# Performance work log

Hardware: AMD Instinct MI355X
Metric: run time of the kernel (lower is better)

The kernel has to match this reference:

```python
import jax, jax.numpy as jnp
import numpy as np

S = 128           # seq_len
B = 256           # input_bits (bits per token, also neurons per head)
H = 16            # num_heads
NB = 12           # n_bits_per_neuron -> LUT size 2^12
PB = 7            # relative-position bits = ceil(log2(max_seq_len))
HEAD_IN = 2 * B + PB   # concat(query, key, rel_pos_bits) = 519
THRESH = H // 2


def setup_inputs() -> dict:
    key = jax.random.key(0)
    k1, k2, k3 = jax.random.split(key, 3)
    tokens = jax.random.randint(k1, (S, B), 0, 2, dtype=jnp.int32)           # binary token bits
    memory = jax.random.normal(k2, (H, B, 2 ** NB), dtype=jnp.float32)       # RAM LUT contents per head/neuron
    connections = jax.random.randint(k3, (H, B, NB), 0, HEAD_IN, dtype=jnp.int32)  # per-neuron input-bit wiring
    return {"tokens": tokens, "memory": memory, "connections": connections}


def reference(tokens, memory, connections):
    idx = jnp.arange(S)
    rel = idx[:, None] - idx[None, :]                         # [S,S] i - j
    mask = (rel >= 0).astype(jnp.int32)                        # causal mask (j <= i)
    relc = jnp.clip(rel, 0, S - 1)
    # relative-distance binary encoding, LSB first: [S,S,PB]
    pos_bits = ((relc[..., None] >> jnp.arange(PB)) & 1).astype(jnp.int32)
    q = jnp.broadcast_to(tokens[:, None, :], (S, S, B))
    k = jnp.broadcast_to(tokens[None, :, :], (S, S, B))
    head_in = jnp.concatenate([q, k, pos_bits], axis=-1)       # [S,S,HEAD_IN]
    # RAM address per (query i, key j, head h, neuron n): pack NB wired bits, LSB first
    addr = jnp.zeros((S, S, H, B), dtype=jnp.int32)
    for b in range(NB):  # tiny fixed loop over bit planes, fully vectorized over S,S,H,B
        addr = addr + (head_in[..., connections[:, :, b]] << b)
    # LUT gather: memory[h, n, addr] -> [S,S,H,B]
    h_idx = jnp.arange(H)[:, None]
    n_idx = jnp.arange(B)[None, :]
    vals = memory[h_idx, n_idx, addr]
    bits = (vals > 0.0).astype(jnp.int32)                      # RAM neuron output bit
    # XOR accumulation over attended keys == masked sum mod 2: [S,H,B]
    head_res = jnp.sum(bits * mask[:, :, None, None], axis=1) % 2
    # majority vote across heads per bit
    ones_count = jnp.sum(head_res, axis=1)                     # [S,B]
    return (ones_count > THRESH).astype(jnp.int32)
```

## Files before the change

### kernel.cpp

```cpp
#include <hip/hip_runtime.h>
#include <hip/hip_bf16.h>


#define S 128
#define B 256
#define H 16
#define NB 12

typedef __attribute__((address_space(3))) void       lds_void;
typedef const __attribute__((address_space(1))) void glb_void;

__device__ __forceinline__ void async16(const float* g, float* l) {
    __builtin_amdgcn_global_load_lds((glb_void*)g, (lds_void*)l, 16, 0, 0);
}

__global__ __launch_bounds__(1024) void softram_kernel(
    const int* __restrict__ tokens,
    const float* __restrict__ memory,
    const int* __restrict__ connections,
    int* __restrict__ out)
{
    const int n    = blockIdx.x;
    const int tid  = threadIdx.x;
    const int wv   = tid >> 6;
    const int lane = tid & 63;

    __shared__ float          raw[2][2][4096];
    __shared__ unsigned int   tok[S * 8];
    __shared__ unsigned short aqs[H][S];
    __shared__ unsigned short aks[H][S];
    __shared__ unsigned short aps[H][S];
    __shared__ int            conns[H][NB];
    __shared__ int            hasP[H];
    __shared__ unsigned char  partsA[H][8];
    __shared__ unsigned char  partsB[H][8];

    auto issue_round = [&](int r, int buf) {
        #pragma unroll
        for (int q2 = 0; q2 < 2; ++q2) {
            int c = wv * 2 + q2;
            const float* g = memory + ((size_t)((2 * r + (c >> 4)) * 256 + n) << 12)
                           + ((c & 15) << 8) + (lane << 2);
            float* l = &raw[buf][c >> 4][(c & 15) << 8];
            async16(g, l);
        }
    };

    issue_round(0, 0);
    {
        int i = tid >> 3, w = tid & 7;
        const int4* tp = (const int4*)tokens;
        unsigned int t = 0;
        #pragma unroll
        for (int u = 0; u < 8; ++u) {
            int4 x = tp[i * 64 + w * 8 + u];
            t |= (unsigned)(x.x & 1) << (4 * u + 0);
            t |= (unsigned)(x.y & 1) << (4 * u + 1);
            t |= (unsigned)(x.z & 1) << (4 * u + 2);
            t |= (unsigned)(x.w & 1) << (4 * u + 3);
        }
        tok[tid] = t;
    }
    if (tid < H * NB) {
        int h = tid / NB, b = tid - h * NB;
        conns[h][b] = connections[h * (B * NB) + n * NB + b];
    }
    __syncthreads();

    issue_round(1, 1);

    if (tid < H) {
        int f = 0;
        #pragma unroll
        for (int b = 0; b < NB; ++b) f |= (conns[tid][b] >= 512);
        hasP[tid] = f;
    }
    #pragma unroll
    for (int e0 = 0; e0 < 2; ++e0) {
        int e = tid + (e0 << 10);
        int h = e >> 7, ii = e & 127;
        unsigned aq = 0, ak = 0, ap = 0;
        #pragma unroll
        for (int b = 0; b < NB; ++b) {
            int c = conns[h][b];
            if (c < 256) {
                aq |= ((tok[ii * 8 + (c >> 5)] >> (c & 31)) & 1u) << b;
            } else if (c < 512) {
                int c2 = c - 256;
                ak |= ((tok[ii * 8 + (c2 >> 5)] >> (c2 & 31)) & 1u) << b;
            } else {
                ap |= (unsigned)((ii >> (c - 512)) & 1) << b;
            }
        }
        aqs[h][ii] = (unsigned short)aq;
        aks[h][ii] = (unsigned short)ak;
        aps[h][ii] = (unsigned short)ap;
    }
    __syncthreads();

    const int hh = wv & 1;
    const int q  = wv >> 1;
    for (int r = 0; r < 8; ++r) {
        if (r < 7) issue_round(r + 1, (r + 1) & 1);

        const int h = 2 * r + hh;
        const float* __restrict__ lrow = &raw[r & 1][hh][0];
        const unsigned ak0 = aks[h][lane];
        const unsigned ak1 = aks[h][lane + 64];
        const bool hp = (hasP[h] != 0);
        unsigned accA = 0, accB = 0;

        {
            uint4 aqw = *(const uint4*)&aqs[h][q * 8];
            const unsigned short* aqp = (const unsigned short*)&aqw;
            #pragma unroll
            for (int t = 0; t < 8; ++t) {
                int i = q * 8 + t;
                unsigned ap0 = hp ? (unsigned)aps[h][(i - lane) & 127] : 0u;
                float v0 = lrow[aqp[t] + ak0 + ap0];
                unsigned long long m0 = __ballot(v0 > 0.0f);
                unsigned long long c0 = (2ull << i) - 1;
                accA |= (unsigned)(__popcll(m0 & c0) & 1) << t;
            }
        }
        {
            uint4 aqw = *(const uint4*)&aqs[h][64 + q * 8];
            const unsigned short* aqp = (const unsigned short*)&aqw;
            #pragma unroll
            for (int t = 0; t < 8; ++t) {
                int i = 64 + q * 8 + t;
                unsigned ap0 = 0, ap1 = 0;
                if (hp) {
                    ap0 = aps[h][(i - lane) & 127];
                    ap1 = aps[h][(i - lane - 64) & 127];
                }
                float v0 = lrow[aqp[t] + ak0 + ap0];
                float v1 = lrow[aqp[t] + ak1 + ap1];
                unsigned long long m0 = __ballot(v0 > 0.0f);
                unsigned long long m1 = __ballot(v1 > 0.0f);
                unsigned long long c1 = (2ull << (i - 64)) - 1;
                accB |= (unsigned)((__popcll(m0) + __popcll(m1 & c1)) & 1) << t;
            }
        }
        if (lane == 0) {
            partsA[h][q] = (unsigned char)accA;
            partsB[h][q] = (unsigned char)accB;
        }
        __syncthreads();
    }

    if (tid < S) {
        int i = tid;
        int tot = 0;
        #pragma unroll
        for (int h2 = 0; h2 < H; ++h2) {
            unsigned bits = (i < 64) ? partsA[h2][i >> 3] : partsB[h2][(i - 64) >> 3];
            tot += (bits >> (i & 7)) & 1;
        }
        out[i * B + n] = (tot > (H / 2)) ? 1 : 0;
    }
}

extern "C" void kernel_launch(void* const* d_in, const int* in_sizes, int n_in,
                              void* d_out, int out_size, void* d_ws, size_t ws_size,
                              hipStream_t stream) {
    const int*   tokens      = (const int*)d_in[0];
    const float* memory      = (const float*)d_in[1];
    const int*   connections = (const int*)d_in[2];
    int*         out         = (int*)d_out;
    (void)in_sizes; (void)n_in; (void)out_size; (void)d_ws; (void)ws_size;

    softram_kernel<<<B, 1024, 0, stream>>>(tokens, memory, connections, out);
}
```

Measured before the change: 126.2 us.

## Binarize LUT into swizzled byte tables and factor address space when no position bits

Each wave now owns one head and loads that head's full LUT row into registers, thresholding it into a byte table in LDS addressed through a bank-swizzle function. The async double-buffered LDS pipeline and the per-round block barriers go away. When a head has no position bits, the address separates into query and key parts, so the masked XOR sum is computed by enumerating the smaller side's subspace across lanes with running XOR and ballots instead of all i,j pairs. Heads with position bits keep the direct gather. This adds data-dependent branching and more complex index logic.

```diff
diff --git a/kernel.cpp b/kernel.cpp
--- a/kernel.cpp
+++ b/kernel.cpp
@@ -7,11 +7,8 @@
 #define H 16
 #define NB 12
 
-typedef __attribute__((address_space(3))) void       lds_void;
-typedef const __attribute__((address_space(1))) void glb_void;
-
-__device__ __forceinline__ void async16(const float* g, float* l) {
-    __builtin_amdgcn_global_load_lds((glb_void*)g, (lds_void*)l, 16, 0, 0);
+__device__ __forceinline__ unsigned sig(unsigned x) {
+    return x ^ ((x >> 3) & 0x70u) ^ ((x >> 6) & 0x70u);
 }
 
 __global__ __launch_bounds__(1024) void softram_kernel(
@@ -22,141 +19,193 @@
 {
     const int n    = blockIdx.x;
     const int tid  = threadIdx.x;
-    const int wv   = tid >> 6;
+    const int h    = tid >> 6;
     const int lane = tid & 63;
 
-    __shared__ float          raw[2][2][4096];
-    __shared__ unsigned int   tok[S * 8];
-    __shared__ unsigned short aqs[H][S];
-    __shared__ unsigned short aks[H][S];
-    __shared__ unsigned short aps[H][S];
+    __shared__ unsigned char  bytetab[H * 4096];
+    __shared__ unsigned int   tokT[8][S];
+    __shared__ unsigned short aqsig[H][S];
+    __shared__ unsigned short aksig[H][S];
+    __shared__ unsigned short apsig[H][S];
     __shared__ int            conns[H][NB];
-    __shared__ int            hasP[H];
-    __shared__ unsigned char  partsA[H][8];
-    __shared__ unsigned char  partsB[H][8];
-
-    auto issue_round = [&](int r, int buf) {
-        #pragma unroll
-        for (int q2 = 0; q2 < 2; ++q2) {
-            int c = wv * 2 + q2;
-            const float* g = memory + ((size_t)((2 * r + (c >> 4)) * 256 + n) << 12)
-                           + ((c & 15) << 8) + (lane << 2);
-            float* l = &raw[buf][c >> 4][(c & 15) << 8];
-            async16(g, l);
-        }
-    };
-
-    issue_round(0, 0);
+    __shared__ unsigned int   parts[H][4];
+
+    const float4* mrow = (const float4*)(memory + ((size_t)(h * 256 + n) << 12));
+    float4 va[8];
+    #pragma unroll
+    for (int t = 0; t < 8; ++t) va[t] = mrow[lane + 64 * t];
+
     {
         int i = tid >> 3, w = tid & 7;
         const int4* tp = (const int4*)tokens;
-        unsigned int t = 0;
+        unsigned v = 0;
         #pragma unroll
         for (int u = 0; u < 8; ++u) {
             int4 x = tp[i * 64 + w * 8 + u];
-            t |= (unsigned)(x.x & 1) << (4 * u + 0);
-            t |= (unsigned)(x.y & 1) << (4 * u + 1);
-            t |= (unsigned)(x.z & 1) << (4 * u + 2);
-            t |= (unsigned)(x.w & 1) << (4 * u + 3);
-        }
-        tok[tid] = t;
+            v |= (unsigned)(x.x & 1) << (4 * u + 0);
+            v |= (unsigned)(x.y & 1) << (4 * u + 1);
+            v |= (unsigned)(x.z & 1) << (4 * u + 2);
+            v |= (unsigned)(x.w & 1) << (4 * u + 3);
+        }
+        tokT[w][i] = v;
     }
     if (tid < H * NB) {
-        int h = tid / NB, b = tid - h * NB;
-        conns[h][b] = connections[h * (B * NB) + n * NB + b];
-    }
+        int hh = tid / NB, b = tid - hh * NB;
+        conns[hh][b] = connections[hh * (B * NB) + n * NB + b];
+    }
+
+    float4 vb[8];
+    #pragma unroll
+    for (int t = 0; t < 8; ++t) vb[t] = mrow[lane + 64 * (t + 8)];
+
     __syncthreads();
 
-    issue_round(1, 1);
-
-    if (tid < H) {
-        int f = 0;
-        #pragma unroll
-        for (int b = 0; b < NB; ++b) f |= (conns[tid][b] >= 512);
-        hasP[tid] = f;
-    }
-    #pragma unroll
-    for (int e0 = 0; e0 < 2; ++e0) {
-        int e = tid + (e0 << 10);
-        int h = e >> 7, ii = e & 127;
+    unsigned qmask = 0, kmask = 0, pmask = 0;
+    #pragma unroll
+    for (int b = 0; b < NB; ++b) {
+        int c = conns[h][b];
+        qmask |= (unsigned)(c < 256) << b;
+        kmask |= (unsigned)(c >= 256 && c < 512) << b;
+        pmask |= (unsigned)(c >= 512) << b;
+    }
+
+    unsigned char* __restrict__ bt = &bytetab[h << 12];
+    #pragma unroll
+    for (int t = 0; t < 16; ++t) {
+        float4 v = (t < 8) ? va[t] : vb[t - 8];
+        unsigned p = 4u * (unsigned)(lane + 64 * t);
+        unsigned w = (unsigned)(v.x > 0.f)
+                   | ((unsigned)(v.y > 0.f) << 8)
+                   | ((unsigned)(v.z > 0.f) << 16)
+                   | ((unsigned)(v.w > 0.f) << 24);
+        *(unsigned*)&bt[sig(p)] = w;
+    }
+
+    #pragma unroll
+    for (int e = 0; e < 2; ++e) {
+        int ii = lane + 64 * e;
         unsigned aq = 0, ak = 0, ap = 0;
         #pragma unroll
         for (int b = 0; b < NB; ++b) {
             int c = conns[h][b];
             if (c < 256) {
-                aq |= ((tok[ii * 8 + (c >> 5)] >> (c & 31)) & 1u) << b;
+                aq |= ((tokT[c >> 5][ii] >> (c & 31)) & 1u) << b;
             } else if (c < 512) {
                 int c2 = c - 256;
-                ak |= ((tok[ii * 8 + (c2 >> 5)] >> (c2 & 31)) & 1u) << b;
+                ak |= ((tokT[c2 >> 5][ii] >> (c2 & 31)) & 1u) << b;
             } else {
-                ap |= (unsigned)((ii >> (c - 512)) & 1) << b;
-            }
-        }
-        aqs[h][ii] = (unsigned short)aq;
-        aks[h][ii] = (unsigned short)ak;
-        aps[h][ii] = (unsigned short)ap;
-    }
-    __syncthreads();
-
-    const int hh = wv & 1;
-    const int q  = wv >> 1;
-    for (int r = 0; r < 8; ++r) {
-        if (r < 7) issue_round(r + 1, (r + 1) & 1);
-
-        const int h = 2 * r + hh;
-        const float* __restrict__ lrow = &raw[r & 1][hh][0];
-        const unsigned ak0 = aks[h][lane];
-        const unsigned ak1 = aks[h][lane + 64];
-        const bool hp = (hasP[h] != 0);
-        unsigned accA = 0, accB = 0;
-
+                ap |= ((unsigned)(ii >> (c - 512)) & 1u) << b;
+            }
+        }
+        aqsig[h][ii] = (unsigned short)sig(aq);
+        aksig[h][ii] = (unsigned short)sig(ak);
+        apsig[h][ii] = (unsigned short)sig(ap);
+    }
+
+    unsigned long long rlo = 0, rhi = 0;
+
+    if (pmask == 0) {
+        int qb = __popc(qmask), kb = __popc(kmask);
+        bool sideQ = (qb <= kb);
+        unsigned smask = sideQ ? qmask : kmask;
+        int m = sideQ ? qb : kb;
+        unsigned spread = 0;
         {
-            uint4 aqw = *(const uint4*)&aqs[h][q * 8];
-            const unsigned short* aqp = (const unsigned short*)&aqw;
+            unsigned k = (unsigned)lane;
+            #pragma unroll
+            for (int b = 0; b < NB; ++b) {
+                if ((smask >> b) & 1u) { spread |= (k & 1u) << b; k >>= 1; }
+            }
+        }
+        const unsigned spv = sig(spread);
+        const int lim = 1 << m;
+        const bool lv = (lane < lim);
+        const unsigned long long vmask =
+            (lim >= 64) ? ~0ull : ((1ull << lim) - 1ull);
+
+        if (sideQ) {
+            unsigned acc = 0;
+            for (int s8 = 0; s8 < 16; ++s8) {
+                uint4 uq = *(const uint4*)&aqsig[h][s8 * 8];
+                uint4 uk = *(const uint4*)&aksig[h][s8 * 8];
+                #pragma unroll
+                for (int t = 0; t < 8; ++t) {
+                    int j = s8 * 8 + t;
+                    unsigned cwk = ((const unsigned*)&uk)[t >> 1];
+                    unsigned cwq = ((const unsigned*)&uq)[t >> 1];
+                    unsigned akv = (cwk >> ((t & 1) * 16)) & 0xffffu;
+                    unsigned aqv = (cwq >> ((t & 1) * 16)) & 0xffffu;
+                    acc ^= bt[akv ^ spv];
+                    unsigned long long accB = __ballot((acc & 1u) != 0u);
+                    unsigned long long mm   = __ballot(lv && (spv == aqv));
+                    unsigned long long bit  = ((accB & mm & vmask) != 0ull);
+                    if (j < 64) rlo |= bit << j; else rhi |= bit << (j - 64);
+                }
+            }
+        } else {
+            unsigned c = 0;
+            for (int s8 = 0; s8 < 16; ++s8) {
+                uint4 uq = *(const uint4*)&aqsig[h][s8 * 8];
+                uint4 uk = *(const uint4*)&aksig[h][s8 * 8];
+                #pragma unroll
+                for (int t = 0; t < 8; ++t) {
+                    int i = s8 * 8 + t;
+                    unsigned cwk = ((const unsigned*)&uk)[t >> 1];
+                    unsigned cwq = ((const unsigned*)&uq)[t >> 1];
+                    unsigned akv = (cwk >> ((t & 1) * 16)) & 0xffffu;
+                    unsigned aqv = (cwq >> ((t & 1) * 16)) & 0xffffu;
+                    c ^= (unsigned)(lv && (spv == akv));
+                    unsigned sb = bt[aqv ^ spv];
+                    unsigned long long mb = __ballot((c & sb & 1u) != 0u);
+                    unsigned long long bit = (unsigned long long)
+                        (__popcll(mb & vmask) & 1ull);
+                    if (i < 64) rlo |= bit << i; else rhi |= bit << (i - 64);
+                }
+            }
+        }
+    } else {
+        const unsigned ak0 = aksig[h][lane];
+        const unsigned ak1 = aksig[h][lane + 64];
+        for (int s8 = 0; s8 < 16; ++s8) {
+            uint4 uq = *(const uint4*)&aqsig[h][s8 * 8];
             #pragma unroll
             for (int t = 0; t < 8; ++t) {
-                int i = q * 8 + t;
-                unsigned ap0 = hp ? (unsigned)aps[h][(i - lane) & 127] : 0u;
-                float v0 = lrow[aqp[t] + ak0 + ap0];
-                unsigned long long m0 = __ballot(v0 > 0.0f);
-                unsigned long long c0 = (2ull << i) - 1;
-                accA |= (unsigned)(__popcll(m0 & c0) & 1) << t;
-            }
-        }
-        {
-            uint4 aqw = *(const uint4*)&aqs[h][64 + q * 8];
-            const unsigned short* aqp = (const unsigned short*)&aqw;
-            #pragma unroll
-            for (int t = 0; t < 8; ++t) {
-                int i = 64 + q * 8 + t;
-                unsigned ap0 = 0, ap1 = 0;
-                if (hp) {
-                    ap0 = aps[h][(i - lane) & 127];
-                    ap1 = aps[h][(i - lane - 64) & 127];
+                int i = s8 * 8 + t;
+                unsigned cwq = ((const unsigned*)&uq)[t >> 1];
+                unsigned aqv = (cwq >> ((t & 1) * 16)) & 0xffffu;
+                unsigned ap0 = apsig[h][(i - lane) & 127];
+                unsigned v0  = bt[aqv ^ ak0 ^ ap0];
+                unsigned long long m0 = __ballot((v0 & 1u) != 0u);
+                unsigned long long pre0 =
+                    (i >= 63) ? ~0ull : ((2ull << i) - 1ull);
+                unsigned cnt = (unsigned)__popcll(m0 & pre0);
+                if (i >= 64) {
+                    unsigned ap1 = apsig[h][(i - lane - 64) & 127];
+                    unsigned v1  = bt[aqv ^ ak1 ^ ap1];
+                    unsigned long long m1 = __ballot((v1 & 1u) != 0u);
+                    unsigned long long pre1 =
+                        (i >= 127) ? ~0ull : ((2ull << (i - 64)) - 1ull);
+                    cnt += (unsigned)__popcll(m1 & pre1);
                 }
-                float v0 = lrow[aqp[t] + ak0 + ap0];
-                float v1 = lrow[aqp[t] + ak1 + ap1];
-                unsigned long long m0 = __ballot(v0 > 0.0f);
-                unsigned long long m1 = __ballot(v1 > 0.0f);
-                unsigned long long c1 = (2ull << (i - 64)) - 1;
-                accB |= (unsigned)((__popcll(m0) + __popcll(m1 & c1)) & 1) << t;
-            }
-        }
-        if (lane == 0) {
-            partsA[h][q] = (unsigned char)accA;
-            partsB[h][q] = (unsigned char)accB;
-        }
-        __syncthreads();
-    }
+                unsigned long long bit = cnt & 1u;
+                if (i < 64) rlo |= bit << i; else rhi |= bit << (i - 64);
+            }
+        }
+    }
+
+    if (lane == 0) {
+        parts[h][0] = (unsigned)rlo;
+        parts[h][1] = (unsigned)(rlo >> 32);
+        parts[h][2] = (unsigned)rhi;
+        parts[h][3] = (unsigned)(rhi >> 32);
+    }
+    __syncthreads();
 
     if (tid < S) {
-        int i = tid;
-        int tot = 0;
+        int i = tid, tot = 0;
         #pragma unroll
-        for (int h2 = 0; h2 < H; ++h2) {
-            unsigned bits = (i < 64) ? partsA[h2][i >> 3] : partsB[h2][(i - 64) >> 3];
-            tot += (bits >> (i & 7)) & 1;
-        }
+        for (int hh = 0; hh < H; ++hh)
+            tot += (parts[hh][i >> 5] >> (i & 31)) & 1;
         out[i * B + n] = (tot > (H / 2)) ? 1 : 0;
     }
 }
```

Result: faster. 114.2 us (-9.5%).
